# Performance work log

Hardware: AMD Instinct MI355X
Metric: run time of the kernel (lower is better)

## Reference

```python
import jax, jax.numpy as jnp
import numpy as np
import math

N_HEAD = 16

def setup_inputs() -> dict:
    key = jax.random.key(0)
    ks = jax.random.split(key, 8)
    B, S, P, NX = 4, 1024, 128, 1024
    return {
        "x": jax.random.normal(ks[0], (B, S, NX), jnp.float32),
        "M": jax.random.normal(ks[1], (B, P, NX), jnp.float32),
        "Mmask": jnp.ones((B, P), jnp.float32),
        "attention_mask": jnp.zeros((B, 1, 1, S), jnp.float32),
        "W_attn": jax.random.normal(ks[2], (NX, 3 * NX), jnp.float32) * 0.02,
        "b_attn": jnp.zeros((3 * NX,), jnp.float32),
        "W_mem": jax.random.normal(ks[3], (NX, 2 * NX), jnp.float32) * 0.02,
        "b_mem": jnp.zeros((2 * NX,), jnp.float32),
        "W_proj": jax.random.normal(ks[4], (NX, NX), jnp.float32) * 0.02,
        "b_proj": jnp.zeros((NX,), jnp.float32),
    }

def _split_heads(t, H):
    B, T, NX = t.shape
    return t.reshape(B, T, H, NX // H).transpose(0, 2, 1, 3)  # [B,H,T,dh]

def reference(x, M, Mmask, attention_mask, W_attn, b_attn, W_mem, b_mem, W_proj, b_proj):
    B, S, NX = x.shape
    H = N_HEAD
    dh = NX // H
    P = M.shape[1]

    # fused QKV projection (Conv1D == x @ W + b)
    qkv = x @ W_attn + b_attn
    q, k, v = jnp.split(qkv, 3, axis=2)

    # memory K/V projection, prepended along the key/value sequence axis
    ekv = M @ W_mem + b_mem
    ek, ev = jnp.split(ekv, 2, axis=2)
    key = jnp.concatenate([ek, k], axis=1)   # [B, P+S, NX]
    value = jnp.concatenate([ev, v], axis=1)

    qh = _split_heads(q, H)      # [B,H,S,dh]
    kh = _split_heads(key, H)    # [B,H,P+S,dh]
    vh = _split_heads(value, H)  # [B,H,P+S,dh]

    w = jnp.einsum('bhsd,bhtd->bhst', qh, kh) / math.sqrt(dh)  # [B,H,S,P+S]

    # causal bias over the self part, all-ones over the memory part
    causal = jnp.tril(jnp.ones((S, S), w.dtype))
    b = jnp.concatenate([jnp.ones((S, P), w.dtype), causal], axis=1)[None, None]  # [1,1,S,P+S]
    w = w * b - 10000.0 * (1.0 - b)

    # additive attention mask: memory-mask bias concatenated before token mask
    mem_bias = (1.0 - Mmask)[:, None, None, :] * -10000.0  # [B,1,1,P]
    am = jnp.concatenate([mem_bias, jnp.broadcast_to(attention_mask, (B, 1, 1, S))], axis=3)
    w = w + am

    w = jax.nn.softmax(w, axis=-1)
    a = jnp.einsum('bhst,bhtd->bhsd', w, vh)                  # [B,H,S,dh]
    a = a.transpose(0, 2, 1, 3).reshape(B, S, NX)             # merge heads
    return a @ W_proj + b_proj
```

## Files before the change

### kernel.cpp

```cpp
#include <hip/hip_runtime.h>
#include <hip/hip_bf16.h>


typedef __attribute__((ext_vector_type(8))) short bf16x8;
typedef __attribute__((ext_vector_type(4))) float f32x4;

#define MFMA16(a, b, c) __builtin_amdgcn_mfma_f32_16x16x32_bf16((a), (b), (c), 0, 0, 0)

#define GLOAD_LDS16(g, l)                                                  \
    __builtin_amdgcn_global_load_lds(                                      \
        (const __attribute__((address_space(1))) void*)(const void*)(g),   \
        (__attribute__((address_space(3))) void*)(void*)(l), 16, 0, 0)

static __device__ __forceinline__ unsigned short f2bf(float f) {
    union { float f; unsigned int u; } v; v.f = f;
    unsigned int u = v.u;
    return (unsigned short)((u + 0x7fffu + ((u >> 16) & 1u)) >> 16);
}

static __device__ __forceinline__ void transpose64(const float* __restrict__ W,
                                                   unsigned short* __restrict__ Wt,
                                                   int K, int N, int bx, int by,
                                                   float* tile ) {
    const int n0 = bx * 64, k0 = by * 64;
    const int tr = threadIdx.x >> 2, tc = (threadIdx.x & 3) * 16;
    #pragma unroll
    for (int i = 0; i < 4; i++) {
        float4 v = *(const float4*)&W[(size_t)(k0 + tr) * N + n0 + tc + i * 4];
        tile[tr * 65 + tc + i * 4 + 0] = v.x;
        tile[tr * 65 + tc + i * 4 + 1] = v.y;
        tile[tr * 65 + tc + i * 4 + 2] = v.z;
        tile[tr * 65 + tc + i * 4 + 3] = v.w;
    }
    __syncthreads();
    union { ushort4 u4[2]; unsigned short s[8]; } pk[2];
    #pragma unroll
    for (int half = 0; half < 2; half++)
        #pragma unroll
        for (int i = 0; i < 8; i++)
            pk[half].s[i] = f2bf(tile[(tc + half * 8 + i) * 65 + tr]);
    unsigned short* dst = &Wt[(size_t)(n0 + tr) * K + k0 + tc];
    *(ushort4*)(dst + 0) = pk[0].u4[0];
    *(ushort4*)(dst + 4) = pk[0].u4[1];
    *(ushort4*)(dst + 8) = pk[1].u4[0];
    *(ushort4*)(dst + 12) = pk[1].u4[1];
}

__global__ void prep_all(const float* __restrict__ x, const float* __restrict__ Mem,
                         unsigned short* __restrict__ x_bf, unsigned short* __restrict__ M_bf,
                         const float* __restrict__ W_attn, const float* __restrict__ W_mem,
                         const float* __restrict__ W_proj, unsigned short* __restrict__ Wat,
                         unsigned short* __restrict__ Wmt, unsigned short* __restrict__ Wpt,
                         const float* __restrict__ Mmask, const float* __restrict__ amask,
                         float* __restrict__ biasT) {
    __shared__ float tile[64 * 65];
    int bid = blockIdx.x;
    if (bid < 4608) {
        int i = bid * 256 + threadIdx.x;
        if (i < 1048576) {
            float4 v = ((const float4*)x)[i];
            ushort4 o; o.x = f2bf(v.x); o.y = f2bf(v.y); o.z = f2bf(v.z); o.w = f2bf(v.w);
            ((ushort4*)x_bf)[i] = o;
        } else {
            int j = i - 1048576;
            float4 v = ((const float4*)Mem)[j];
            ushort4 o; o.x = f2bf(v.x); o.y = f2bf(v.y); o.z = f2bf(v.z); o.w = f2bf(v.w);
            ((ushort4*)M_bf)[j] = o;
        }
        return;
    }
    bid -= 4608;
    if (bid < 768) {
        transpose64(W_attn, Wat, 1024, 3072, bid % 48, bid / 48, tile);
    } else if (bid < 1280) {
        int t = bid - 768;  transpose64(W_mem, Wmt, 1024, 2048, t % 32, t / 32, tile);
    } else if (bid < 1536) {
        int t = bid - 1280; transpose64(W_proj, Wpt, 1024, 1024, t % 16, t / 16, tile);
    } else {
        int i = (bid - 1536) * 256 + threadIdx.x;
        if (i < 4 * 1152) {
            int b = i / 1152, t = i % 1152;
            float v = (t < 128) ? (Mmask[b * 128 + t] - 1.f) * 10000.f
                                : amask[b * 1024 + t - 128];
            biasT[i] = v * 1.4426950408889634f;
        }
    }
}

__global__ __launch_bounds__(512, 2) void gemm_fused(
        const unsigned short* __restrict__ x_bf, const unsigned short* __restrict__ Wat,
        const float* __restrict__ b_attn, const unsigned short* __restrict__ M_bf,
        const unsigned short* __restrict__ Wmt, const float* __restrict__ b_mem,
        unsigned short* __restrict__ Qbuf, unsigned short* __restrict__ Kc,
        unsigned short* __restrict__ Vt) {
    __shared__ unsigned short lds[2][32768];
    const int tid = threadIdx.x;
    const int lane = tid & 63, wave = tid >> 6;
    const int quad = lane >> 4, l16 = lane & 15;
    const int l7 = l16 & 7;
    const int srow = lane >> 3;
    const int sblk = (lane & 7) ^ srow;
    const int wrow = wave * 16;
    const int wm = (wave & 1) * 128;
    const int wn = (wave >> 1) * 64;

    int tm, tn;
    const unsigned short *Ab, *Bb;
    const float* bias;
    bool qkv;
    if (blockIdx.x < 192) {
        const int nb = (blockIdx.x & 7) * 24 + (blockIdx.x >> 3);
        tm = nb & 15; tn = nb >> 4;
        Ab = x_bf; Bb = Wat; bias = b_attn; qkv = true;
    } else {
        const int e = blockIdx.x - 192;
        tm = e >> 3; tn = e & 7;
        Ab = M_bf; Bb = Wmt; bias = b_mem; qkv = false;
    }
    const int Mrow0 = tm * 256, Nrow0 = tn * 256;

#define STG(slot, dstoff, srcp, row0, kt1)                                     \
    { _Pragma("unroll")                                                        \
      for (int c = 0; c < 2; c++)                                              \
          GLOAD_LDS16((srcp) + (size_t)((row0) + wrow + c * 8 + srow) * 1024 + \
                          (kt1) * 64 + sblk * 8,                               \
                      &lds[slot][(dstoff) + (wrow + c * 8) * 64]); }

    STG(0, 16384, Bb, Nrow0, 0); STG(0, 24576, Bb, Nrow0 + 128, 0);
    STG(0, 0,     Ab, Mrow0, 0); STG(0, 8192,  Ab, Mrow0 + 128, 0);
    asm volatile("s_waitcnt vmcnt(0)\n\ts_barrier" ::: "memory");

    f32x4 acc[8][4] = {};
    for (int kt = 0; kt < 16; kt++) {
        const int s = kt & 1, nx = s ^ 1;
        bf16x8 bfr[4][2];
        #pragma unroll
        for (int p = 0; p < 4; p++) {
            bf16x8 af[2][2];
            #pragma unroll
            for (int k = 0; k < 2; k++)
                #pragma unroll
                for (int ks = 0; ks < 2; ks++)
                    af[k][ks] = *(const bf16x8*)&lds[s][(wm + (2 * p + k) * 16 + l16) * 64 +
                                                       (((ks * 4 + quad) ^ l7) * 8)];
            if (p == 0) {
                #pragma unroll
                for (int j = 0; j < 4; j++)
                    #pragma unroll
                    for (int ks = 0; ks < 2; ks++)
                        bfr[j][ks] = *(const bf16x8*)&lds[s][16384 + (wn + j * 16 + l16) * 64 +
                                                            (((ks * 4 + quad) ^ l7) * 8)];
            }
            if (kt < 15) {
                if (p == 0) { STG(nx, 16384, Bb, Nrow0, kt + 1);
                              STG(nx, 24576, Bb, Nrow0 + 128, kt + 1); }
                else if (p == 1) { STG(nx, 0,    Ab, Mrow0, kt + 1); }
                else if (p == 2) { STG(nx, 8192, Ab, Mrow0 + 128, kt + 1); }
            }
            if (p == 3) asm volatile("s_waitcnt vmcnt(0)\n\ts_barrier" ::: "memory");
            else        asm volatile("s_barrier" ::: "memory");
            __builtin_amdgcn_s_setprio(1);
            #pragma unroll
            for (int k = 0; k < 2; k++)
                #pragma unroll
                for (int j = 0; j < 4; j++) {
                    acc[2 * p + k][j] = MFMA16(af[k][0], bfr[j][0], acc[2 * p + k][j]);
                    acc[2 * p + k][j] = MFMA16(af[k][1], bfr[j][1], acc[2 * p + k][j]);
                }
            __builtin_amdgcn_s_setprio(0);
            asm volatile("s_barrier" ::: "memory");
        }
    }
#undef STG
    __syncthreads();

    float bj[4];
    #pragma unroll
    for (int j = 0; j < 4; j++) bj[j] = bias[Nrow0 + wn + j * 16 + l16];

    if (qkv) {
        const int b = tm >> 2;
        const int sb = (tm & 3) * 256 + wm;
        if (tn < 4) {
            #pragma unroll
            for (int i = 0; i < 8; i++) {
                const int row = Mrow0 + wm + i * 16 + quad * 4;
                #pragma unroll
                for (int j = 0; j < 4; j++) {
                    const int col = Nrow0 + wn + j * 16 + l16;
                    #pragma unroll
                    for (int r = 0; r < 4; r++)
                        Qbuf[(size_t)(row + r) * 1024 + col] = f2bf(acc[i][j][r] + bj[j]);
                }
            }
        } else if (tn < 8) {
            const int cb = (tn - 4) * 256 + wn;
            unsigned short* kb2 = Kc + (size_t)((b << 4) | (cb >> 6)) * 73728;
            #pragma unroll
            for (int i = 0; i < 8; i++) {
                const int s0 = sb + i * 16 + quad * 4;
                #pragma unroll
                for (int j = 0; j < 4; j++) {
                    const int d = j * 16 + l16;
                    #pragma unroll
                    for (int r = 0; r < 4; r++)
                        kb2[(size_t)(128 + s0 + r) * 64 + d] = f2bf(acc[i][j][r] + bj[j]);
                }
            }
        } else {
            const int vb = (tn - 8) * 256 + wn;
            unsigned short* Tw = &lds[0][0] + wave * 4352;
            unsigned short* vdb = Vt + (size_t)((b << 4) | (vb >> 6)) * 73728;
            #pragma unroll
            for (int hf = 0; hf < 2; hf++) {
                #pragma unroll
                for (int i2 = 0; i2 < 4; i2++)
                    #pragma unroll
                    for (int j = 0; j < 4; j++)
                        #pragma unroll
                        for (int r = 0; r < 4; r++)
                            Tw[(j * 16 + l16) * 68 + i2 * 16 + quad * 4 + r] =
                                f2bf(acc[hf * 4 + i2][j][r] + bj[j]);
                unsigned short* vd = vdb + (size_t)lane * 1152 + 128 + sb + hf * 64;
                #pragma unroll
                for (int ch = 0; ch < 8; ch++)
                    *(bf16x8*)(vd + ch * 8) = *(const bf16x8*)&Tw[lane * 68 + ch * 8];
            }
        }
    } else {
        const int b = (Mrow0 + wm) >> 7;
        if (tn < 4) {
            const int cb = tn * 256 + wn;
            unsigned short* kb2 = Kc + (size_t)((b << 4) | (cb >> 6)) * 73728;
            #pragma unroll
            for (int i = 0; i < 8; i++) {
                const int p0 = i * 16 + quad * 4;
                #pragma unroll
                for (int j = 0; j < 4; j++) {
                    const int d = j * 16 + l16;
                    #pragma unroll
                    for (int r = 0; r < 4; r++)
                        kb2[(size_t)(p0 + r) * 64 + d] = f2bf(acc[i][j][r] + bj[j]);
                }
            }
        } else {
            const int vb = (tn - 4) * 256 + wn;
            unsigned short* Tw = &lds[0][0] + wave * 4352;
            unsigned short* vdb = Vt + (size_t)((b << 4) | (vb >> 6)) * 73728;
            #pragma unroll
            for (int hf = 0; hf < 2; hf++) {
                #pragma unroll
                for (int i2 = 0; i2 < 4; i2++)
                    #pragma unroll
                    for (int j = 0; j < 4; j++)
                        #pragma unroll
                        for (int r = 0; r < 4; r++)
                            Tw[(j * 16 + l16) * 68 + i2 * 16 + quad * 4 + r] =
                                f2bf(acc[hf * 4 + i2][j][r] + bj[j]);
                unsigned short* vd = vdb + (size_t)lane * 1152 + hf * 64;
                #pragma unroll
                for (int ch = 0; ch < 8; ch++)
                    *(bf16x8*)(vd + ch * 8) = *(const bf16x8*)&Tw[lane * 68 + ch * 8];
            }
        }
    }
}

__global__ __launch_bounds__(128) void attn_kernel(const unsigned short* __restrict__ Qbuf,
                                                   const unsigned short* __restrict__ Kc,
                                                   const unsigned short* __restrict__ Vt,
                                                   const float* __restrict__ biasT,
                                                   unsigned short* __restrict__ Aout) {
    __shared__ unsigned short Ks[2][64 * 64];
    __shared__ unsigned short Vs[2][64 * 64];
    __shared__ unsigned short Ps[2][16 * 72];
    const int tid = threadIdx.x;
    const int lane = tid & 63, wave = tid >> 6;
    const int quad = lane >> 4, l16 = lane & 15;
    const int blk = blockIdx.x;
    const int xcd = blk & 7, idx = blk >> 3;
    const int bh = xcd * 8 + (idx & 7);
    const int pair = idx >> 3;
    const int h = bh & 15, b = bh >> 4;

    const unsigned short* Kb = Kc + (size_t)bh * 73728;
    const unsigned short* Vb = Vt + (size_t)bh * 73728;
    const float* bias_b = biasT + b * 1152;

    const int srow = lane >> 3;
    const int scol = ((lane & 7) ^ srow) * 8;
    const int rswz = l16 & 7;
    const int w32 = wave * 32;

#define STAGE_KV(t0_, kdst_, vdst_)                                            \
    {                                                                          \
        const unsigned short* gk = Kb + (size_t)((t0_) + w32 + srow) * 64 + scol; \
        const unsigned short* gv = Vb + (size_t)(w32 + srow) * 1152 + (t0_) + scol; \
        _Pragma("unroll")                                                      \
        for (int cc = 0; cc < 4; cc++) {                                       \
            GLOAD_LDS16(gk + (size_t)(cc * 8) * 64,   &(kdst_)[(w32 + cc * 8) * 64]); \
            GLOAD_LDS16(gv + (size_t)(cc * 8) * 1152, &(vdst_)[(w32 + cc * 8) * 64]); \
        }                                                                      \
    }

    bf16x8 ones;
    #pragma unroll
    for (int j = 0; j < 8; j++) ones[j] = (short)0x3F80;

    #pragma unroll
    for (int phase = 0; phase < 2; phase++) {
        const int qg = phase ? (31 - pair) : pair;
        const int qrow0 = qg * 32;
        const int qrow_w = qrow0 + wave * 16;

        bf16x8 qf[2];
        #pragma unroll
        for (int k2 = 0; k2 < 2; k2++)
            qf[k2] = *(const bf16x8*)(Qbuf + (size_t)(b * 1024 + qrow_w + l16) * 1024 +
                                      h * 64 + k2 * 32 + quad * 8);

        f32x4 o[4] = {};
        f32x4 oden = {};
        const int tmax = min(1152, ((qrow0 + 223) >> 6) << 6);

        STAGE_KV(0, Ks[0], Vs[0]);

        for (int t0 = 0; t0 < tmax; t0 += 64) {
            const int cur = (t0 >> 6) & 1;
            if (t0 + 64 < tmax) {
                if (cur) { STAGE_KV(t0 + 64, Ks[0], Vs[0]); }
                else     { STAGE_KV(t0 + 64, Ks[1], Vs[1]); }
                asm volatile("s_waitcnt vmcnt(8)\n\ts_barrier" ::: "memory");
            } else {
                asm volatile("s_waitcnt vmcnt(0)\n\ts_barrier" ::: "memory");
            }
            if (t0 <= qrow_w + 143) {
                const unsigned short* Kcur = Ks[cur];
                const unsigned short* Vcur = Vs[cur];
                const bool nomask = (t0 + 63 <= 128 + qrow_w);
                float4 bt[4];
                #pragma unroll
                for (int tn = 0; tn < 4; tn++)
                    bt[tn] = *(const float4*)(bias_b + t0 + tn * 16 + quad * 4);
                const int sg = qrow_w + l16;
                #pragma unroll
                for (int tn = 0; tn < 4; tn++) {
                    bf16x8 kf0 = *(const bf16x8*)&Kcur[(tn * 16 + l16) * 64 + (quad ^ rswz) * 8];
                    bf16x8 kf1 = *(const bf16x8*)&Kcur[(tn * 16 + l16) * 64 + ((quad + 4) ^ rswz) * 8];
                    f32x4 st = {};
                    st = MFMA16(kf0, qf[0], st);
                    st = MFMA16(kf1, qf[1], st);
                    float p[4];
                    #pragma unroll
                    for (int r = 0; r < 4; r++) {
                        float e = __builtin_amdgcn_exp2f(st[r] * 0.18033688011112042f + bt[tn][r]);
                        if (!nomask) {
                            const int tg = t0 + tn * 16 + quad * 4 + r;
                            e = (tg < 128 || tg - 128 <= sg) ? e : 0.f;
                        }
                        p[r] = e;
                    }
                    union { ushort4 u; __hip_bfloat162 h2[2]; } pk;
                    pk.h2[0] = __float22bfloat162_rn(float2{p[0], p[1]});
                    pk.h2[1] = __float22bfloat162_rn(float2{p[2], p[3]});
                    *(ushort4*)&Ps[wave][l16 * 72 + tn * 16 + quad * 4] = pk.u;
                }
                #pragma unroll
                for (int tk = 0; tk < 2; tk++) {
                    bf16x8 pf = *(const bf16x8*)&Ps[wave][l16 * 72 + tk * 32 + quad * 8];
                    oden = MFMA16(pf, ones, oden);
                    #pragma unroll
                    for (int dn = 0; dn < 4; dn++) {
                        bf16x8 vf = *(const bf16x8*)&Vcur[(dn * 16 + l16) * 64 +
                                                          ((tk * 4 + quad) ^ rswz) * 8];
                        o[dn] = MFMA16(pf, vf, o[dn]);
                    }
                }
            }
            asm volatile("s_barrier" ::: "memory");
        }

        #pragma unroll
        for (int r = 0; r < 4; r++) {
            const float inv = 1.f / oden[r];
            const size_t orow = (size_t)(b * 1024 + qrow_w + quad * 4 + r) * 1024 + h * 64;
            #pragma unroll
            for (int dn = 0; dn < 4; dn++)
                Aout[orow + dn * 16 + l16] = f2bf(o[dn][r] * inv);
        }
    }
#undef STAGE_KV
}

__global__ __launch_bounds__(256) void gemm_proj(const unsigned short* __restrict__ Abuf,
                                                 const unsigned short* __restrict__ Wpt,
                                                 const float* __restrict__ b_proj,
                                                 float* __restrict__ out) {
    __shared__ unsigned short As[128 * 32];
    __shared__ unsigned short Bs[64 * 32];
    const int tid = threadIdx.x;
    const int lane = tid & 63, wave = tid >> 6;
    const int quad = lane >> 4, l16 = lane & 15;
    const int wm = (wave & 1) * 64, wn = (wave >> 1) * 32;
    const int bm = blockIdx.x & 31, bn = blockIdx.x >> 5;
    const int crow = lane >> 2, ccol = (lane & 3) * 8;
    const unsigned short* Abase = Abuf + (size_t)(bm * 128 + crow) * 1024 + ccol;
    const unsigned short* Bbase = Wpt + (size_t)(bn * 64 + crow) * 1024 + ccol;

    f32x4 acc[4][2] = {};
    for (int k0 = 0; k0 < 1024; k0 += 32) {
        __syncthreads();
        #pragma unroll
        for (int cc = 0; cc < 3; cc++) {
            const int c = wave * 3 + cc;
            if (c < 8) GLOAD_LDS16(Abase + (size_t)(c * 16) * 1024 + k0, &As[c * 512]);
            else if (c < 12) GLOAD_LDS16(Bbase + (size_t)((c - 8) * 16) * 1024 + k0, &Bs[(c - 8) * 512]);
        }
        __syncthreads();
        bf16x8 af[4], bf[2];
        #pragma unroll
        for (int i = 0; i < 4; i++) af[i] = *(const bf16x8*)&As[(wm + i * 16 + l16) * 32 + quad * 8];
        #pragma unroll
        for (int j = 0; j < 2; j++) bf[j] = *(const bf16x8*)&Bs[(wn + j * 16 + l16) * 32 + quad * 8];
        #pragma unroll
        for (int i = 0; i < 4; i++)
            #pragma unroll
            for (int j = 0; j < 2; j++)
                acc[i][j] = MFMA16(af[i], bf[j], acc[i][j]);
    }
    float bj[2];
    #pragma unroll
    for (int j = 0; j < 2; j++) bj[j] = b_proj[bn * 64 + wn + j * 16 + l16];
    #pragma unroll
    for (int i = 0; i < 4; i++) {
        const int row = bm * 128 + wm + i * 16 + quad * 4;
        #pragma unroll
        for (int j = 0; j < 2; j++) {
            const int col = bn * 64 + wn + j * 16 + l16;
            #pragma unroll
            for (int r = 0; r < 4; r++)
                out[(size_t)(row + r) * 1024 + col] = acc[i][j][r] + bj[j];
        }
    }
}

extern "C" void kernel_launch(void* const* d_in, const int* in_sizes, int n_in,
                              void* d_out, int out_size, void* d_ws, size_t ws_size,
                              hipStream_t stream) {
    const float* x      = (const float*)d_in[0];
    const float* Mem    = (const float*)d_in[1];
    const float* Mmask  = (const float*)d_in[2];
    const float* amask  = (const float*)d_in[3];
    const float* W_attn = (const float*)d_in[4];
    const float* b_attn = (const float*)d_in[5];
    const float* W_mem  = (const float*)d_in[6];
    const float* b_mem  = (const float*)d_in[7];
    const float* W_proj = (const float*)d_in[8];
    const float* b_proj = (const float*)d_in[9];
    float* out = (float*)d_out;

    char* ws = (char*)d_ws;
    unsigned short* x_bf  = (unsigned short*)ws;  ws += (size_t)4096 * 1024 * 2;
    unsigned short* M_bf  = (unsigned short*)ws;  ws += (size_t)512 * 1024 * 2;
    unsigned short* Wat   = (unsigned short*)ws;  ws += (size_t)3072 * 1024 * 2;
    unsigned short* Wmt   = (unsigned short*)ws;  ws += (size_t)2048 * 1024 * 2;
    unsigned short* Wpt   = (unsigned short*)ws;  ws += (size_t)1024 * 1024 * 2;
    unsigned short* Qbuf  = (unsigned short*)ws;  ws += (size_t)4096 * 1024 * 2;
    unsigned short* Abuf  = (unsigned short*)ws;  ws += (size_t)4096 * 1024 * 2;
    unsigned short* Kc    = (unsigned short*)ws;  ws += (size_t)64 * 1152 * 64 * 2;
    unsigned short* Vt    = (unsigned short*)ws;  ws += (size_t)64 * 64 * 1152 * 2;
    float*          biasT = (float*)ws;           ws += (size_t)4 * 1152 * 4;

    prep_all<<<6163, 256, 0, stream>>>(x, Mem, x_bf, M_bf, W_attn, W_mem, W_proj,
                                       Wat, Wmt, Wpt, Mmask, amask, biasT);
    gemm_fused<<<208, 512, 0, stream>>>(x_bf, Wat, b_attn, M_bf, Wmt, b_mem,
                                        Qbuf, Kc, Vt);
    attn_kernel<<<1024, 128, 0, stream>>>(Qbuf, Kc, Vt, biasT, Abuf);
    gemm_proj<<<512, 256, 0, stream>>>(Abuf, Wpt, b_proj, out);
}
```

Measured before the change: 197.8 us.

## Prefetch two k-tiles ahead and double-buffer A fragments in QKV GEMM

Restructures the projection GEMM main loop so global-to-LDS loads run two k-tiles ahead, waiting with vmcnt(8) instead of draining all loads every tile. Inside a tile, A fragments are register double-buffered so the next group's LDS reads overlap the current MFMAs. The per-subgroup barriers are removed, leaving two per tile. The aim is to hide global-load latency and reduce synchronisation stalls, at the cost of more registers for the extra A fragment buffer. The wait-then-refill of the slot just consumed also places a barrier and a vmcnt wait directly on the load path.

```diff
diff --git a/kernel.cpp b/kernel.cpp
--- a/kernel.cpp
+++ b/kernel.cpp
@@ -126,51 +126,61 @@
                           (kt1) * 64 + sblk * 8,                               \
                       &lds[slot][(dstoff) + (wrow + c * 8) * 64]); }
 
-    STG(0, 16384, Bb, Nrow0, 0); STG(0, 24576, Bb, Nrow0 + 128, 0);
-    STG(0, 0,     Ab, Mrow0, 0); STG(0, 8192,  Ab, Mrow0 + 128, 0);
-    asm volatile("s_waitcnt vmcnt(0)\n\ts_barrier" ::: "memory");
+#define STG_KT(slot, kt1)                                                      \
+    { STG(slot, 16384, Bb, Nrow0, kt1); STG(slot, 24576, Bb, Nrow0 + 128, kt1);\
+      STG(slot, 0,     Ab, Mrow0, kt1); STG(slot, 8192,  Ab, Mrow0 + 128, kt1); }
+
+    STG_KT(0, 0);
+    STG_KT(1, 1);
+    asm volatile("s_waitcnt vmcnt(8)\n\ts_barrier" ::: "memory");
 
     f32x4 acc[8][4] = {};
     for (int kt = 0; kt < 16; kt++) {
-        const int s = kt & 1, nx = s ^ 1;
-        bf16x8 bfr[4][2];
-        #pragma unroll
-        for (int p = 0; p < 4; p++) {
-            bf16x8 af[2][2];
+        const int s = kt & 1;
+        bf16x8 bfr[4][2], af[2][2][2];
+        #pragma unroll
+        for (int j = 0; j < 4; j++)
+            #pragma unroll
+            for (int ks = 0; ks < 2; ks++)
+                bfr[j][ks] = *(const bf16x8*)&lds[s][16384 + (wn + j * 16 + l16) * 64 +
+                                                    (((ks * 4 + quad) ^ l7) * 8)];
+        #pragma unroll
+        for (int k = 0; k < 2; k++)
+            #pragma unroll
+            for (int ks = 0; ks < 2; ks++)
+                af[0][k][ks] = *(const bf16x8*)&lds[s][(wm + k * 16 + l16) * 64 +
+                                                       (((ks * 4 + quad) ^ l7) * 8)];
+        #pragma unroll
+        for (int g = 0; g < 4; g++) {
+            const int cb = g & 1, nb2 = cb ^ 1;
+            if (g < 3) {
+                #pragma unroll
+                for (int k = 0; k < 2; k++)
+                    #pragma unroll
+                    for (int ks = 0; ks < 2; ks++)
+                        af[nb2][k][ks] = *(const bf16x8*)&lds[s][
+                            (wm + ((g + 1) * 2 + k) * 16 + l16) * 64 +
+                            (((ks * 4 + quad) ^ l7) * 8)];
+            }
+            __builtin_amdgcn_s_setprio(1);
             #pragma unroll
             for (int k = 0; k < 2; k++)
                 #pragma unroll
-                for (int ks = 0; ks < 2; ks++)
-                    af[k][ks] = *(const bf16x8*)&lds[s][(wm + (2 * p + k) * 16 + l16) * 64 +
-                                                       (((ks * 4 + quad) ^ l7) * 8)];
-            if (p == 0) {
-                #pragma unroll
-                for (int j = 0; j < 4; j++)
-                    #pragma unroll
-                    for (int ks = 0; ks < 2; ks++)
-                        bfr[j][ks] = *(const bf16x8*)&lds[s][16384 + (wn + j * 16 + l16) * 64 +
-                                                            (((ks * 4 + quad) ^ l7) * 8)];
-            }
-            if (kt < 15) {
-                if (p == 0) { STG(nx, 16384, Bb, Nrow0, kt + 1);
-                              STG(nx, 24576, Bb, Nrow0 + 128, kt + 1); }
-                else if (p == 1) { STG(nx, 0,    Ab, Mrow0, kt + 1); }
-                else if (p == 2) { STG(nx, 8192, Ab, Mrow0 + 128, kt + 1); }
-            }
-            if (p == 3) asm volatile("s_waitcnt vmcnt(0)\n\ts_barrier" ::: "memory");
-            else        asm volatile("s_barrier" ::: "memory");
-            __builtin_amdgcn_s_setprio(1);
-            #pragma unroll
-            for (int k = 0; k < 2; k++)
-                #pragma unroll
                 for (int j = 0; j < 4; j++) {
-                    acc[2 * p + k][j] = MFMA16(af[k][0], bfr[j][0], acc[2 * p + k][j]);
-                    acc[2 * p + k][j] = MFMA16(af[k][1], bfr[j][1], acc[2 * p + k][j]);
+                    acc[g * 2 + k][j] = MFMA16(af[cb][k][0], bfr[j][0], acc[g * 2 + k][j]);
+                    acc[g * 2 + k][j] = MFMA16(af[cb][k][1], bfr[j][1], acc[g * 2 + k][j]);
                 }
             __builtin_amdgcn_s_setprio(0);
-            asm volatile("s_barrier" ::: "memory");
-        }
-    }
+        }
+        asm volatile("s_waitcnt lgkmcnt(0)\n\ts_barrier" ::: "memory");
+        if (kt < 14) {
+            STG_KT(s, kt + 2);
+            asm volatile("s_waitcnt vmcnt(8)\n\ts_barrier" ::: "memory");
+        } else {
+            asm volatile("s_waitcnt vmcnt(0)\n\ts_barrier" ::: "memory");
+        }
+    }
+#undef STG_KT
 #undef STG
     __syncthreads();
 
```

Result: no change. 200.7 us (+1.4%).

## Drop KV double buffering and phase pairing; launch one query group per block

Applied to the files above, without the earlier changes.

The attention kernel now uses single-buffered K/V tiles loaded between two block barriers, instead of prefetching the next tile into a second buffer. Each block handles one 32-row query group rather than a balanced pair of short and long causal groups, and the grid doubles. The XCD-aware head mapping is replaced by a simple modulo mapping. Halving LDS may let more blocks reside per CU, but load latency is no longer overlapped within a block, and causal work imbalance is left to the hardware scheduler.

```diff
diff --git a/kernel.cpp b/kernel.cpp
--- a/kernel.cpp
+++ b/kernel.cpp
@@ -271,16 +271,15 @@
                                                    const unsigned short* __restrict__ Vt,
                                                    const float* __restrict__ biasT,
                                                    unsigned short* __restrict__ Aout) {
-    __shared__ unsigned short Ks[2][64 * 64];
-    __shared__ unsigned short Vs[2][64 * 64];
+    __shared__ unsigned short Ks[64 * 64];
+    __shared__ unsigned short Vs[64 * 64];
     __shared__ unsigned short Ps[2][16 * 72];
     const int tid = threadIdx.x;
     const int lane = tid & 63, wave = tid >> 6;
     const int quad = lane >> 4, l16 = lane & 15;
     const int blk = blockIdx.x;
-    const int xcd = blk & 7, idx = blk >> 3;
-    const int bh = xcd * 8 + (idx & 7);
-    const int pair = idx >> 3;
+    const int bh = blk & 63;
+    const int qg = blk >> 6;
     const int h = bh & 15, b = bh >> 4;
 
     const unsigned short* Kb = Kc + (size_t)bh * 73728;
@@ -292,104 +291,86 @@
     const int rswz = l16 & 7;
     const int w32 = wave * 32;
 
-#define STAGE_KV(t0_, kdst_, vdst_)                                            \
-    {                                                                          \
-        const unsigned short* gk = Kb + (size_t)((t0_) + w32 + srow) * 64 + scol; \
-        const unsigned short* gv = Vb + (size_t)(w32 + srow) * 1152 + (t0_) + scol; \
-        _Pragma("unroll")                                                      \
-        for (int cc = 0; cc < 4; cc++) {                                       \
-            GLOAD_LDS16(gk + (size_t)(cc * 8) * 64,   &(kdst_)[(w32 + cc * 8) * 64]); \
-            GLOAD_LDS16(gv + (size_t)(cc * 8) * 1152, &(vdst_)[(w32 + cc * 8) * 64]); \
-        }                                                                      \
-    }
-
     bf16x8 ones;
     #pragma unroll
     for (int j = 0; j < 8; j++) ones[j] = (short)0x3F80;
 
-    #pragma unroll
-    for (int phase = 0; phase < 2; phase++) {
-        const int qg = phase ? (31 - pair) : pair;
-        const int qrow0 = qg * 32;
-        const int qrow_w = qrow0 + wave * 16;
-
-        bf16x8 qf[2];
-        #pragma unroll
-        for (int k2 = 0; k2 < 2; k2++)
-            qf[k2] = *(const bf16x8*)(Qbuf + (size_t)(b * 1024 + qrow_w + l16) * 1024 +
-                                      h * 64 + k2 * 32 + quad * 8);
-
-        f32x4 o[4] = {};
-        f32x4 oden = {};
-        const int tmax = min(1152, ((qrow0 + 223) >> 6) << 6);
-
-        STAGE_KV(0, Ks[0], Vs[0]);
-
-        for (int t0 = 0; t0 < tmax; t0 += 64) {
-            const int cur = (t0 >> 6) & 1;
-            if (t0 + 64 < tmax) {
-                if (cur) { STAGE_KV(t0 + 64, Ks[0], Vs[0]); }
-                else     { STAGE_KV(t0 + 64, Ks[1], Vs[1]); }
-                asm volatile("s_waitcnt vmcnt(8)\n\ts_barrier" ::: "memory");
-            } else {
-                asm volatile("s_waitcnt vmcnt(0)\n\ts_barrier" ::: "memory");
-            }
-            if (t0 <= qrow_w + 143) {
-                const unsigned short* Kcur = Ks[cur];
-                const unsigned short* Vcur = Vs[cur];
-                const bool nomask = (t0 + 63 <= 128 + qrow_w);
-                float4 bt[4];
-                #pragma unroll
-                for (int tn = 0; tn < 4; tn++)
-                    bt[tn] = *(const float4*)(bias_b + t0 + tn * 16 + quad * 4);
-                const int sg = qrow_w + l16;
-                #pragma unroll
-                for (int tn = 0; tn < 4; tn++) {
-                    bf16x8 kf0 = *(const bf16x8*)&Kcur[(tn * 16 + l16) * 64 + (quad ^ rswz) * 8];
-                    bf16x8 kf1 = *(const bf16x8*)&Kcur[(tn * 16 + l16) * 64 + ((quad + 4) ^ rswz) * 8];
-                    f32x4 st = {};
-                    st = MFMA16(kf0, qf[0], st);
-                    st = MFMA16(kf1, qf[1], st);
-                    float p[4];
-                    #pragma unroll
-                    for (int r = 0; r < 4; r++) {
-                        float e = __builtin_amdgcn_exp2f(st[r] * 0.18033688011112042f + bt[tn][r]);
-                        if (!nomask) {
-                            const int tg = t0 + tn * 16 + quad * 4 + r;
-                            e = (tg < 128 || tg - 128 <= sg) ? e : 0.f;
-                        }
-                        p[r] = e;
+    const int qrow0 = qg * 32;
+    const int qrow_w = qrow0 + wave * 16;
+
+    bf16x8 qf[2];
+    #pragma unroll
+    for (int k2 = 0; k2 < 2; k2++)
+        qf[k2] = *(const bf16x8*)(Qbuf + (size_t)(b * 1024 + qrow_w + l16) * 1024 +
+                                  h * 64 + k2 * 32 + quad * 8);
+
+    f32x4 o[4] = {};
+    f32x4 oden = {};
+    const int tmax = min(1152, ((qrow0 + 223) >> 6) << 6);
+    const int sg = qrow_w + l16;
+
+    for (int t0 = 0; t0 < tmax; t0 += 64) {
+        __syncthreads();
+        {
+            const unsigned short* gk = Kb + (size_t)(t0 + w32 + srow) * 64 + scol;
+            const unsigned short* gv = Vb + (size_t)(w32 + srow) * 1152 + t0 + scol;
+            #pragma unroll
+            for (int cc = 0; cc < 4; cc++) {
+                GLOAD_LDS16(gk + (size_t)(cc * 8) * 64,   &Ks[(w32 + cc * 8) * 64]);
+                GLOAD_LDS16(gv + (size_t)(cc * 8) * 1152, &Vs[(w32 + cc * 8) * 64]);
+            }
+        }
+        __syncthreads();
+        if (t0 <= qrow_w + 143) {
+            const bool nomask = (t0 + 63 <= 128 + qrow_w);
+            float4 bt[4];
+            #pragma unroll
+            for (int tn = 0; tn < 4; tn++)
+                bt[tn] = *(const float4*)(bias_b + t0 + tn * 16 + quad * 4);
+            #pragma unroll
+            for (int tn = 0; tn < 4; tn++) {
+                bf16x8 kf0 = *(const bf16x8*)&Ks[(tn * 16 + l16) * 64 + (quad ^ rswz) * 8];
+                bf16x8 kf1 = *(const bf16x8*)&Ks[(tn * 16 + l16) * 64 + ((quad + 4) ^ rswz) * 8];
+                f32x4 st = {};
+                st = MFMA16(kf0, qf[0], st);
+                st = MFMA16(kf1, qf[1], st);
+                float p[4];
+                #pragma unroll
+                for (int r = 0; r < 4; r++) {
+                    float e = __builtin_amdgcn_exp2f(st[r] * 0.18033688011112042f + bt[tn][r]);
+                    if (!nomask) {
+                        const int tg = t0 + tn * 16 + quad * 4 + r;
+                        e = (tg < 128 || tg - 128 <= sg) ? e : 0.f;
                     }
-                    union { ushort4 u; __hip_bfloat162 h2[2]; } pk;
-                    pk.h2[0] = __float22bfloat162_rn(float2{p[0], p[1]});
-                    pk.h2[1] = __float22bfloat162_rn(float2{p[2], p[3]});
-                    *(ushort4*)&Ps[wave][l16 * 72 + tn * 16 + quad * 4] = pk.u;
-                }
-                #pragma unroll
-                for (int tk = 0; tk < 2; tk++) {
-                    bf16x8 pf = *(const bf16x8*)&Ps[wave][l16 * 72 + tk * 32 + quad * 8];
-                    oden = MFMA16(pf, ones, oden);
-                    #pragma unroll
-                    for (int dn = 0; dn < 4; dn++) {
-                        bf16x8 vf = *(const bf16x8*)&Vcur[(dn * 16 + l16) * 64 +
-                                                          ((tk * 4 + quad) ^ rswz) * 8];
-                        o[dn] = MFMA16(pf, vf, o[dn]);
-                    }
-                }
-            }
-            asm volatile("s_barrier" ::: "memory");
-        }
-
-        #pragma unroll
-        for (int r = 0; r < 4; r++) {
-            const float inv = 1.f / oden[r];
-            const size_t orow = (size_t)(b * 1024 + qrow_w + quad * 4 + r) * 1024 + h * 64;
-            #pragma unroll
-            for (int dn = 0; dn < 4; dn++)
-                Aout[orow + dn * 16 + l16] = f2bf(o[dn][r] * inv);
-        }
-    }
-#undef STAGE_KV
+                    p[r] = e;
+                }
+                union { ushort4 u; __hip_bfloat162 h2[2]; } pk;
+                pk.h2[0] = __float22bfloat162_rn(float2{p[0], p[1]});
+                pk.h2[1] = __float22bfloat162_rn(float2{p[2], p[3]});
+                *(ushort4*)&Ps[wave][l16 * 72 + tn * 16 + quad * 4] = pk.u;
+            }
+            #pragma unroll
+            for (int tk = 0; tk < 2; tk++) {
+                bf16x8 pf = *(const bf16x8*)&Ps[wave][l16 * 72 + tk * 32 + quad * 8];
+                oden = MFMA16(pf, ones, oden);
+                #pragma unroll
+                for (int dn = 0; dn < 4; dn++) {
+                    bf16x8 vf = *(const bf16x8*)&Vs[(dn * 16 + l16) * 64 +
+                                                    ((tk * 4 + quad) ^ rswz) * 8];
+                    o[dn] = MFMA16(pf, vf, o[dn]);
+                }
+            }
+        }
+    }
+
+    #pragma unroll
+    for (int r = 0; r < 4; r++) {
+        const float inv = 1.f / oden[r];
+        const size_t orow = (size_t)(b * 1024 + qrow_w + quad * 4 + r) * 1024 + h * 64;
+        #pragma unroll
+        for (int dn = 0; dn < 4; dn++)
+            Aout[orow + dn * 16 + l16] = f2bf(o[dn][r] * inv);
+    }
 }
 
 __global__ __launch_bounds__(256) void gemm_proj(const unsigned short* __restrict__ Abuf,
@@ -475,6 +456,6 @@
                                        Wat, Wmt, Wpt, Mmask, amask, biasT);
     gemm_fused<<<208, 512, 0, stream>>>(x_bf, Wat, b_attn, M_bf, Wmt, b_mem,
                                         Qbuf, Kc, Vt);
-    attn_kernel<<<1024, 128, 0, stream>>>(Qbuf, Kc, Vt, biasT, Abuf);
+    attn_kernel<<<2048, 128, 0, stream>>>(Qbuf, Kc, Vt, biasT, Abuf);
     gemm_proj<<<512, 256, 0, stream>>>(Abuf, Wpt, b_proj, out);
 }
```

Result: no change. 199.3 us (+0.7%).
